# Kernel optimization log

Measured on AMD Instinct MI355X. Metric: run time of the kernel, lower is better.

## Reference

```python
import jax, jax.numpy as jnp
import numpy as np

D_MODEL = 768
D_STATE = 16
D_CONV = 4
EXPAND = 2
N_LAYERS = 8
VOCAB = 512
MAXSEQ = 2048
BATCH = 8
SEQ = 2048
D_INNER = EXPAND * D_MODEL
N_EMO, N_STY, N_KEY, N_MODE = 8, 8, 12, 2


def setup_inputs() -> dict:
    key = jax.random.key(0)
    ks = jax.random.split(key, 32)
    def nrm(k, shape, s=0.02):
        return (jax.random.normal(k, shape) * s).astype(jnp.float32)
    inp = {}
    inp['tokens'] = jax.random.randint(ks[0], (BATCH, SEQ), 0, VOCAB)
    inp['emotion'] = jax.random.randint(ks[1], (BATCH,), 0, N_EMO)
    inp['style'] = jax.random.randint(ks[2], (BATCH,), 0, N_STY)
    inp['key_sig'] = jax.random.randint(ks[3], (BATCH,), 0, N_KEY)
    inp['mode'] = jax.random.randint(ks[4], (BATCH,), 0, N_MODE)
    inp['bpm'] = (jax.random.uniform(ks[5], (BATCH,)) * 140.0 + 60.0).astype(jnp.float32)
    inp['tok_emb'] = nrm(ks[6], (VOCAB, D_MODEL))
    inp['emo_emb'] = nrm(ks[7], (N_EMO, D_MODEL))
    inp['sty_emb'] = nrm(ks[8], (N_STY, D_MODEL))
    inp['key_emb'] = nrm(ks[9], (N_KEY, D_MODEL))
    inp['mode_emb'] = nrm(ks[10], (N_MODE, D_MODEL))
    inp['bpm_w'] = nrm(ks[11], (D_MODEL, 1))
    inp['bpm_b'] = jnp.zeros((D_MODEL,), jnp.float32)
    inp['cond_w'] = nrm(ks[12], (D_MODEL, 5 * D_MODEL))
    inp['cond_b'] = jnp.zeros((D_MODEL,), jnp.float32)
    inp['pos_emb'] = nrm(ks[13], (MAXSEQ, D_MODEL))
    inp['ln_g'] = jnp.ones((N_LAYERS, D_MODEL), jnp.float32)
    inp['ln_b'] = jnp.zeros((N_LAYERS, D_MODEL), jnp.float32)
    inp['in_w'] = nrm(ks[14], (N_LAYERS, 2 * D_INNER, D_MODEL))
    inp['conv_w'] = nrm(ks[15], (N_LAYERS, D_INNER, 1, D_CONV), 0.1)
    inp['xproj_w'] = nrm(ks[16], (N_LAYERS, 2 * D_STATE, D_INNER))
    inp['dt_w'] = nrm(ks[17], (N_LAYERS, D_INNER, D_STATE))
    inp['dt_b'] = jnp.zeros((N_LAYERS, D_INNER), jnp.float32)
    inp['bproj_w'] = nrm(ks[18], (N_LAYERS, D_INNER, D_STATE))
    inp['d_param'] = jnp.ones((N_LAYERS, D_INNER), jnp.float32)
    inp['out_w'] = nrm(ks[19], (N_LAYERS, D_MODEL, D_INNER))
    inp['final_g'] = jnp.ones((D_MODEL,), jnp.float32)
    inp['final_b'] = jnp.zeros((D_MODEL,), jnp.float32)
    inp['head_w'] = nrm(ks[20], (VOCAB, D_MODEL))
    inp['head_b'] = jnp.zeros((VOCAB,), jnp.float32)
    return inp


def _layernorm(x, g, b):
    mu = x.mean(-1, keepdims=True)
    v = ((x - mu) ** 2).mean(-1, keepdims=True)
    return (x - mu) * jax.lax.rsqrt(v + 1e-5) * g + b


def _silu(x):
    return x * jax.nn.sigmoid(x)


def _mamba_block(x, in_w, conv_w, xproj_w, dt_w, dt_b, bproj_w, d_param, out_w):
    B, L, _ = x.shape
    xz = x @ in_w.T                       # [B,L,2*di]
    xc, z = jnp.split(xz, 2, axis=-1)
    # causal depthwise conv1d: torch pads d_conv-1 both sides then slices [:L]
    xt = jnp.transpose(xc, (0, 2, 1))     # [B,di,L]
    xt = jax.lax.conv_general_dilated(xt, conv_w, (1,), [(D_CONV - 1, 0)],
                                      feature_group_count=D_INNER)
    xc = _silu(jnp.transpose(xt, (0, 2, 1)))   # [B,L,di]
    dt_raw, b_raw = jnp.split(xc @ xproj_w.T, 2, axis=-1)  # each [B,L,ds]
    delta = jnp.clip(jax.nn.softplus(dt_raw @ dt_w.T + dt_b), 1e-4, 1.0)  # [B,L,di]
    bp = b_raw @ bproj_w.T                 # [B,L,di]

    def step(h, inputs):
        d, u, bb = inputs
        h = h * (1.0 - d) + u * bb
        return h, h

    xs = (jnp.transpose(delta, (1, 0, 2)),
          jnp.transpose(xc, (1, 0, 2)),
          jnp.transpose(bp, (1, 0, 2)))    # time-major [L,B,di]
    h0 = jnp.zeros((B, D_INNER), x.dtype)
    _, ys = jax.lax.scan(step, h0, xs)
    y = jnp.transpose(ys, (1, 0, 2)) + d_param * xc
    y = y * _silu(z)
    return y @ out_w.T


def reference(tokens, emotion, style, key_sig, mode, bpm, tok_emb, emo_emb, sty_emb,
              key_emb, mode_emb, bpm_w, bpm_b, cond_w, cond_b, pos_emb, ln_g, ln_b,
              in_w, conv_w, xproj_w, dt_w, dt_b, bproj_w, d_param, out_w,
              final_g, final_b, head_w, head_b):
    B, L = tokens.shape
    cond = jnp.concatenate([
        emo_emb[emotion], sty_emb[style], key_emb[key_sig], mode_emb[mode],
        bpm[:, None] @ bpm_w.T + bpm_b], axis=-1)       # [B,5d]
    cond = cond @ cond_w.T + cond_b                      # [B,d]
    x = tok_emb[tokens] + cond[:, None, :] + pos_emb[:L][None]
    for i in range(N_LAYERS):
        res = x
        h = _layernorm(x, ln_g[i], ln_b[i])
        x = res + _mamba_block(h, in_w[i], conv_w[i], xproj_w[i], dt_w[i],
                               dt_b[i], bproj_w[i], d_param[i], out_w[i])
    x = _layernorm(x, final_g, final_b)
    return x @ head_w.T + head_b
```

## Files before the change

kernel.cpp:

```cpp
#include <hip/hip_runtime.h>
#include <cstdint>

#define BATCH 8
#define SEQ   2048
#define DM    768
#define DI    1536
#define DS    16
#define NL    8
#define NVOCAB 512
#define BT    (BATCH*SEQ)
#define NCHUNK 32
#define TC    (SEQ/NCHUNK)

typedef __attribute__((ext_vector_type(8))) short bf16x8;
typedef __attribute__((ext_vector_type(4))) float f32x4;

__device__ __forceinline__ unsigned short f2bf(float f){
  unsigned int u = __float_as_uint(f);
  u += 0x7fffu + ((u >> 16) & 1u);
  return (unsigned short)(u >> 16);
}
__device__ __forceinline__ float bf2f(unsigned short s){
  return __uint_as_float(((unsigned int)s) << 16);
}
__device__ __forceinline__ float sigm(float x){ return 1.0f/(1.0f + __expf(-x)); }
__device__ __forceinline__ float siluf(float x){ return x * sigm(x); }
__device__ __forceinline__ float fast_softplus(float x){
  return (x > 15.0f) ? x : __logf(1.0f + __expf(x));
}
__device__ __forceinline__ void async16(void* l, const void* g){
  __builtin_amdgcn_global_load_lds(
      (const __attribute__((address_space(1))) unsigned int*)g,
      (__attribute__((address_space(3))) unsigned int*)l, 16, 0, 0);
}
__device__ __forceinline__ float dot4(f32x4 a, f32x4 b){
  return fmaf(a[0],b[0], fmaf(a[1],b[1], fmaf(a[2],b[2], a[3]*b[3])));
}

__global__ void cvt_bf16_kernel(const float4* __restrict__ in, ushort4* __restrict__ out, int n4){
  int i = blockIdx.x*256 + threadIdx.x;
  int stride = gridDim.x*256;
  for(; i<n4; i+=stride){
    float4 v = in[i];
    ushort4 o; o.x=f2bf(v.x); o.y=f2bf(v.y); o.z=f2bf(v.z); o.w=f2bf(v.w);
    out[i]=o;
  }
}

__global__ void wcomb_kernel(const float* __restrict__ dt_w, const float* __restrict__ bproj_w,
                             unsigned short* __restrict__ out){
  int idx = blockIdx.x*256 + threadIdx.x;
  int k = idx & 31, ld = idx >> 5;
  float v = (k < 16) ? dt_w[(long)ld*16 + k] : bproj_w[(long)ld*16 + (k-16)];
  out[idx] = f2bf(v);
}

__global__ __launch_bounds__(256) void cond_kernel(const int* __restrict__ emotion,
    const int* __restrict__ style, const int* __restrict__ keysig, const int* __restrict__ modei,
    const float* __restrict__ bpm, const float* __restrict__ emo_emb, const float* __restrict__ sty_emb,
    const float* __restrict__ key_emb, const float* __restrict__ mode_emb,
    const float* __restrict__ bpm_w, const float* __restrict__ bpm_b,
    const float* __restrict__ cond_w, const float* __restrict__ cond_b,
    float* __restrict__ cond_out){
  int b = blockIdx.y;
  int tid = threadIdx.x;
  __shared__ float vec[5*DM];
  int e = emotion[b], st = style[b], ks = keysig[b], md = modei[b];
  float bp = bpm[b];
  for(int j=tid; j<960; j+=256){
    int seg = j/192, o4 = j - seg*192;
    float4 v;
    if(seg==0)      v = reinterpret_cast<const float4*>(emo_emb + (long)e*DM)[o4];
    else if(seg==1) v = reinterpret_cast<const float4*>(sty_emb + (long)st*DM)[o4];
    else if(seg==2) v = reinterpret_cast<const float4*>(key_emb + (long)ks*DM)[o4];
    else if(seg==3) v = reinterpret_cast<const float4*>(mode_emb + (long)md*DM)[o4];
    else {
      float4 w = reinterpret_cast<const float4*>(bpm_w)[o4];
      float4 bb = reinterpret_cast<const float4*>(bpm_b)[o4];
      v = make_float4(fmaf(bp,w.x,bb.x), fmaf(bp,w.y,bb.y), fmaf(bp,w.z,bb.z), fmaf(bp,w.w,bb.w));
    }
    reinterpret_cast<float4*>(vec)[j] = v;
  }
  __syncthreads();
  int wid = tid>>6, lane = tid&63;
  int dm = blockIdx.x*4 + wid;
  const float4* w4 = reinterpret_cast<const float4*>(cond_w + (long)dm*(5*DM));
  const float4* v4 = reinterpret_cast<const float4*>(vec);
  float acc = 0.f;
  #pragma unroll 5
  for(int j=lane; j<960; j+=64){
    float4 w = w4[j], v = v4[j];
    acc = fmaf(w.x,v.x, fmaf(w.y,v.y, fmaf(w.z,v.z, fmaf(w.w,v.w, acc))));
  }
  #pragma unroll
  for(int off=32; off>0; off>>=1) acc += __shfl_xor(acc, off);
  if(lane==0) cond_out[b*DM + dm] = acc + cond_b[dm];
}

__global__ void embed_kernel(const int* __restrict__ tokens, const float* __restrict__ tok_emb,
    const float* __restrict__ cond, const float* __restrict__ pos_emb, float* __restrict__ x){
  int bt = blockIdx.x;
  int b = bt >> 11, t = bt & 2047;
  int tok = tokens[bt];
  const float4* te = reinterpret_cast<const float4*>(tok_emb + (long)tok*DM);
  const float4* ce = reinterpret_cast<const float4*>(cond + (long)b*DM);
  const float4* pe = reinterpret_cast<const float4*>(pos_emb + (long)t*DM);
  float4* xo = reinterpret_cast<float4*>(x + (long)bt*DM);
  int i = threadIdx.x;
  float4 a = te[i], c = ce[i], p = pe[i];
  xo[i] = make_float4(a.x+c.x+p.x, a.y+c.y+p.y, a.z+c.z+p.z, a.w+c.w+p.w);
}

__global__ __launch_bounds__(256) void ln_bf16_kernel(const float* __restrict__ x,
                     const float* __restrict__ g, const float* __restrict__ bta,
                     unsigned short* __restrict__ out){
  int row  = blockIdx.x*4 + (threadIdx.x >> 6);
  int lane = threadIdx.x & 63;
  const float* xr = x + (long)row*DM;
  float4 v[3];
  float sum=0.f, sq=0.f;
  #pragma unroll
  for(int i=0;i<3;i++){
    v[i] = *reinterpret_cast<const float4*>(xr + i*256 + lane*4);
    sum += v[i].x + v[i].y + v[i].z + v[i].w;
    sq  += v[i].x*v[i].x + v[i].y*v[i].y + v[i].z*v[i].z + v[i].w*v[i].w;
  }
  #pragma unroll
  for(int off=32; off>0; off>>=1){
    sum += __shfl_xor(sum, off);
    sq  += __shfl_xor(sq , off);
  }
  float mu  = sum * (1.0f/DM);
  float var = sq  * (1.0f/DM) - mu*mu;
  float rs  = rsqrtf(var + 1e-5f);
  unsigned short* orow = out + (long)row*DM;
  #pragma unroll
  for(int i=0;i<3;i++){
    int d = i*256 + lane*4;
    float4 gg = *reinterpret_cast<const float4*>(g + d);
    float4 bb = *reinterpret_cast<const float4*>(bta + d);
    ushort4 o;
    o.x = f2bf((v[i].x - mu)*rs*gg.x + bb.x);
    o.y = f2bf((v[i].y - mu)*rs*gg.y + bb.y);
    o.z = f2bf((v[i].z - mu)*rs*gg.z + bb.z);
    o.w = f2bf((v[i].w - mu)*rs*gg.w + bb.w);
    *reinterpret_cast<ushort4*>(orow + d) = o;
  }
}

template<int MODE>
__global__ __launch_bounds__(256) void gemm_lds(const unsigned short* __restrict__ A,
                                               const unsigned short* __restrict__ B,
                                               void* __restrict__ Cv,
                                               const float* __restrict__ bias,
                                               int K, int ldc){
  __shared__ short As[128*64];
  __shared__ short Bs[128*64];
  const short* Ap = (const short*)A;
  const short* Bp = (const short*)B;
  int tid  = threadIdx.x;
  int lane = tid & 63;
  int wid  = tid >> 6;

  int nbx = gridDim.x;
  int id  = blockIdx.y*nbx + blockIdx.x;
  int q   = (nbx*gridDim.y) >> 3;
  int swz = (id & 7)*q + (id >> 3);
  int bx  = swz % nbx, by = swz / nbx;
  int row0 = by*128;
  int col0 = bx*128;

  int srow[4], goff[4];
  #pragma unroll
  for(int j=0;j<4;j++){
    int c = j*256 + tid;
    int row = c>>3, s = c&7;
    srow[j] = row;
    goff[j] = (s ^ (row&7))*8;
  }

  int wr = (wid>>1)*64;
  int wc = (wid&1)*64;
  int fr = lane & 15;
  int kq = lane >> 4;
  int fx = fr & 7;

  f32x4 acc[4][4];
  #pragma unroll
  for(int m=0;m<4;m++)
    #pragma unroll
    for(int n=0;n<4;n++)
      acc[m][n] = (f32x4){0.f,0.f,0.f,0.f};

  for(int kt=0; kt<K; kt+=64){
    #pragma unroll
    for(int j=0;j<4;j++){
      int c = j*256 + tid;
      async16((char*)As + c*16, Ap + (long)(row0+srow[j])*K + kt + goff[j]);
      async16((char*)Bs + c*16, Bp + (long)(col0+srow[j])*K + kt + goff[j]);
    }
    __syncthreads();
    #pragma unroll
    for(int ks=0; ks<2; ks++){
      int sA = ((ks*4 + kq) ^ fx) * 8;
      bf16x8 av[4], bv[4];
      #pragma unroll
      for(int m=0;m<4;m++)
        av[m] = *reinterpret_cast<const bf16x8*>(As + (wr + m*16 + fr)*64 + sA);
      #pragma unroll
      for(int n=0;n<4;n++)
        bv[n] = *reinterpret_cast<const bf16x8*>(Bs + (wc + n*16 + fr)*64 + sA);
      #pragma unroll
      for(int m=0;m<4;m++)
        #pragma unroll
        for(int n=0;n<4;n++)
          acc[m][n] = __builtin_amdgcn_mfma_f32_16x16x32_bf16(av[m], bv[n], acc[m][n], 0, 0, 0);
    }
    __syncthreads();
  }

  int rr = (lane >> 4) << 2;
  int cc = lane & 15;
  #pragma unroll
  for(int m=0;m<4;m++){
    #pragma unroll
    for(int n=0;n<4;n++){
      int col = col0 + wc + n*16 + cc;
      #pragma unroll
      for(int i=0;i<4;i++){
        long idx = (long)(row0 + wr + m*16 + rr + i)*ldc + col;
        float v = acc[m][n][i];
        if(MODE==3)      ((unsigned short*)Cv)[idx] = f2bf(v);
        else if(MODE==1) ((float*)Cv)[idx] += v;
        else if(MODE==2) ((float*)Cv)[idx] = v + bias[col];
        else             ((float*)Cv)[idx] = v;
      }
    }
  }
}

__global__ __launch_bounds__(512) void gemm256(const unsigned short* __restrict__ A,
                                               const unsigned short* __restrict__ B,
                                               unsigned short* __restrict__ C,
                                               int K, int ldc){
  __shared__ short smem[2][2][256*64];
  const short* Ap = (const short*)A;
  const short* Bp = (const short*)B;
  int tid  = threadIdx.x;
  int lane = tid & 63;
  int wid  = tid >> 6;

  int nbx = gridDim.x;
  int id  = blockIdx.y*nbx + blockIdx.x;
  int q   = (nbx*gridDim.y) >> 3;
  int swz = (id & 7)*q + (id >> 3);
  int bx  = swz % nbx, by = swz / nbx;
  int row0 = by*256;
  int col0 = bx*256;

  int srow[4], goff[4];
  #pragma unroll
  for(int j=0;j<4;j++){
    int c = j*512 + tid;
    int row = c>>3, s = c&7;
    srow[j] = row;
    goff[j] = (s ^ (row&7))*8;
  }

  int wr = (wid>>2)*128;
  int wc = (wid&3)*64;
  int fr = lane & 15;
  int kq = lane >> 4;
  int fx = fr & 7;

  f32x4 acc[8][4];
  #pragma unroll
  for(int m=0;m<8;m++)
    #pragma unroll
    for(int n=0;n<4;n++)
      acc[m][n] = (f32x4){0.f,0.f,0.f,0.f};

  #define STAGE256(buf, kt) { \
    char* aB = (char*)&smem[buf][0][0]; \
    char* bB = (char*)&smem[buf][1][0]; \
    _Pragma("unroll") \
    for(int j=0;j<4;j++){ \
      int c = j*512 + tid; \
      async16(aB + c*16, Ap + (long)(row0+srow[j])*K + (kt) + goff[j]); \
      async16(bB + c*16, Bp + (long)(col0+srow[j])*K + (kt) + goff[j]); \
    } }

  int NT = K >> 6;
  STAGE256(0, 0)
  for(int t=0; t<NT; ++t){
    int cur = t & 1;
    if(t+1 < NT){
      STAGE256(cur^1, (t+1)*64)
      asm volatile("s_waitcnt vmcnt(8)" ::: "memory");
    } else {
      asm volatile("s_waitcnt vmcnt(0)" ::: "memory");
    }
    __builtin_amdgcn_s_barrier();
    __builtin_amdgcn_sched_barrier(0);
    const short* As = &smem[cur][0][0];
    const short* Bs = &smem[cur][1][0];
    __builtin_amdgcn_s_setprio(1);
    #pragma unroll
    for(int qp=0; qp<4; qp++){
      int qm = qp>>1, qn = qp&1;
      bf16x8 av[4][2], bv[2][2];
      #pragma unroll
      for(int ks=0; ks<2; ks++){
        int sA = ((ks*4 + kq) ^ fx) * 8;
        #pragma unroll
        for(int m4=0;m4<4;m4++)
          av[m4][ks] = *reinterpret_cast<const bf16x8*>(As + (wr + (qm*4+m4)*16 + fr)*64 + sA);
        #pragma unroll
        for(int n2=0;n2<2;n2++)
          bv[n2][ks] = *reinterpret_cast<const bf16x8*>(Bs + (wc + (qn*2+n2)*16 + fr)*64 + sA);
      }
      #pragma unroll
      for(int ks=0; ks<2; ks++)
        #pragma unroll
        for(int m4=0;m4<4;m4++)
          #pragma unroll
          for(int n2=0;n2<2;n2++)
            acc[qm*4+m4][qn*2+n2] = __builtin_amdgcn_mfma_f32_16x16x32_bf16(
                av[m4][ks], bv[n2][ks], acc[qm*4+m4][qn*2+n2], 0, 0, 0);
    }
    __builtin_amdgcn_s_setprio(0);
    __builtin_amdgcn_sched_barrier(0);
    __builtin_amdgcn_s_barrier();
  }
  #undef STAGE256

  int rr = (lane >> 4) << 2;
  int cc = lane & 15;
  #pragma unroll
  for(int m=0;m<8;m++){
    #pragma unroll
    for(int n=0;n<4;n++){
      int col = col0 + wc + n*16 + cc;
      #pragma unroll
      for(int i=0;i<4;i++){
        long idx = (long)(row0 + wr + m*16 + rr + i)*ldc + col;
        C[idx] = f2bf(acc[m][n][i]);
      }
    }
  }
}

__global__ __launch_bounds__(256) void xproj_kernel(const unsigned short* __restrict__ xz,
      const float* __restrict__ cw, const unsigned short* __restrict__ wbf,
      float* __restrict__ dtb){
  __shared__ unsigned short xcs[16][DI+8];
  __shared__ float pdt[4][16][32];
  int blk = blockIdx.x;
  int b  = blk >> 7;
  int t0 = (blk & 127) << 4;
  int tid = threadIdx.x;
  long base = ((long)b*SEQ + t0)*(2*DI);
  if(tid < 192){
    int d0 = tid*8;
    float cc0[8], cc1[8], cc2[8], cc3[8];
    #pragma unroll
    for(int j=0;j<8;j++){
      cc0[j]=cw[(d0+j)*4+0]; cc1[j]=cw[(d0+j)*4+1];
      cc2[j]=cw[(d0+j)*4+2]; cc3[j]=cw[(d0+j)*4+3];
    }
    float wm3[8], wm2[8], wm1[8];
    #pragma unroll
    for(int j=0;j<8;j++){ wm3[j]=0.f; wm2[j]=0.f; wm1[j]=0.f; }
    if(t0>0){
      bf16x8 v3 = *reinterpret_cast<const bf16x8*>(xz + base - 3*(2*DI) + d0);
      bf16x8 v2 = *reinterpret_cast<const bf16x8*>(xz + base - 2*(2*DI) + d0);
      bf16x8 v1 = *reinterpret_cast<const bf16x8*>(xz + base - 1*(2*DI) + d0);
      #pragma unroll
      for(int j=0;j<8;j++){
        wm3[j]=bf2f((unsigned short)v3[j]);
        wm2[j]=bf2f((unsigned short)v2[j]);
        wm1[j]=bf2f((unsigned short)v1[j]);
      }
    }
    for(int tt=0; tt<16; tt++){
      bf16x8 vt = *reinterpret_cast<const bf16x8*>(xz + base + (long)tt*(2*DI) + d0);
      bf16x8 o;
      #pragma unroll
      for(int j=0;j<8;j++){
        float wt = bf2f((unsigned short)vt[j]);
        float u  = cc0[j]*wm3[j] + cc1[j]*wm2[j] + cc2[j]*wm1[j] + cc3[j]*wt;
        o[j] = (short)f2bf(siluf(u));
        wm3[j]=wm2[j]; wm2[j]=wm1[j]; wm1[j]=wt;
      }
      *reinterpret_cast<bf16x8*>(&xcs[tt][d0]) = o;
    }
  }
  __syncthreads();
  int wid = tid >> 6, lane = tid & 63;
  int fr = lane & 15, kq = lane >> 4;
  f32x4 a0 = (f32x4){0.f,0.f,0.f,0.f};
  f32x4 a1 = (f32x4){0.f,0.f,0.f,0.f};
  const unsigned short* w0 = wbf + (long)fr*DI;
  const unsigned short* w1 = wbf + (long)(16+fr)*DI;
  int kbase = wid*384 + kq*8;
  #pragma unroll
  for(int ks=0; ks<12; ks++){
    int k = kbase + ks*32;
    bf16x8 av = *reinterpret_cast<const bf16x8*>(&xcs[fr][k]);
    bf16x8 b0 = *reinterpret_cast<const bf16x8*>(w0 + k);
    bf16x8 b1 = *reinterpret_cast<const bf16x8*>(w1 + k);
    a0 = __builtin_amdgcn_mfma_f32_16x16x32_bf16(av, b0, a0, 0, 0, 0);
    a1 = __builtin_amdgcn_mfma_f32_16x16x32_bf16(av, b1, a1, 0, 0, 0);
  }
  int rr = kq << 2;
  #pragma unroll
  for(int i=0;i<4;i++){
    pdt[wid][rr+i][fr]      = a0[i];
    pdt[wid][rr+i][16+fr]   = a1[i];
  }
  __syncthreads();
  for(int e = tid; e < 512; e += 256){
    int r = e >> 5, s = e & 31;
    float v = pdt[0][r][s] + pdt[1][r][s] + pdt[2][r][s] + pdt[3][r][s];
    dtb[((long)b*SEQ + t0 + r)*32 + s] = v;
  }
}

__global__ __launch_bounds__(256) void scanAY_mfma_kernel(const unsigned short* __restrict__ xz,
      const float* __restrict__ dtb, const float* __restrict__ cw,
      const unsigned short* __restrict__ wcomb,
      const float* __restrict__ dtbias_g, const float* __restrict__ dp_g,
      float2* __restrict__ chunk, unsigned short* __restrict__ y0s,
      unsigned short* __restrict__ as_s){
  __shared__ unsigned short abuf[64][32];
  __shared__ unsigned short dab[64*256*2];
  int c = blockIdx.x, db = blockIdx.y, b = blockIdx.z;
  int tid = threadIdx.x;
  int t0 = c*TC;
  {
    const float4* src = reinterpret_cast<const float4*>(dtb + ((long)b*SEQ + t0)*32);
    float4 v0 = src[tid*2], v1 = src[tid*2+1];
    bf16x8 o;
    o[0]=(short)f2bf(v0.x); o[1]=(short)f2bf(v0.y); o[2]=(short)f2bf(v0.z); o[3]=(short)f2bf(v0.w);
    o[4]=(short)f2bf(v1.x); o[5]=(short)f2bf(v1.y); o[6]=(short)f2bf(v1.z); o[7]=(short)f2bf(v1.w);
    *reinterpret_cast<bf16x8*>(&abuf[tid>>2][(tid&3)*8]) = o;
  }
  __syncthreads();
  {
    int w = tid >> 6, lane = tid & 63;
    int fr = lane & 15, kq = lane >> 4;
    bf16x8 zero = {0,0,0,0,0,0,0,0};
    bf16x8 bq[4], bp[4];
    #pragma unroll
    for(int nt=0; nt<4; nt++){
      int dcol = db*256 + w*64 + nt*16 + fr;
      bf16x8 wv = *reinterpret_cast<const bf16x8*>(wcomb + (long)dcol*32 + kq*8);
      bq[nt] = (kq<2) ? wv : zero;
      bp[nt] = (kq<2) ? zero : wv;
    }
    #pragma unroll
    for(int mt=0; mt<4; mt++){
      bf16x8 av = *reinterpret_cast<const bf16x8*>(&abuf[mt*16 + fr][kq*8]);
      #pragma unroll
      for(int nt=0; nt<4; nt++){
        f32x4 aq = __builtin_amdgcn_mfma_f32_16x16x32_bf16(av, bq[nt], (f32x4){0.f,0.f,0.f,0.f}, 0,0,0);
        f32x4 ap = __builtin_amdgcn_mfma_f32_16x16x32_bf16(av, bp[nt], (f32x4){0.f,0.f,0.f,0.f}, 0,0,0);
        int dl = w*64 + nt*16 + fr;
        #pragma unroll
        for(int i=0;i<4;i++){
          int t = mt*16 + kq*4 + i;
          unsigned int pack = (unsigned int)f2bf(aq[i]) | (((unsigned int)f2bf(ap[i]))<<16);
          *reinterpret_cast<unsigned int*>(&dab[(t*256 + dl)*2]) = pack;
        }
      }
    }
  }
  int d = db*256 + tid;
  float c0=cw[d*4],c1=cw[d*4+1],c2=cw[d*4+2],c3=cw[d*4+3];
  float bias = dtbias_g[d];
  float dp = dp_g[d];
  asm volatile("" : "+v"(c0),"+v"(c1),"+v"(c2),"+v"(c3),"+v"(bias),"+v"(dp));
  long base = ((long)b*SEQ + t0)*(2*DI) + d;
  float wm3 = (t0>0) ? bf2f(xz[base - 3*(2*DI)]) : 0.f;
  float wm2 = (t0>0) ? bf2f(xz[base - 2*(2*DI)]) : 0.f;
  float wm1 = (t0>0) ? bf2f(xz[base - 1*(2*DI)]) : 0.f;
  const unsigned short* xp = xz + base;
  long sidx = ((long)b*SEQ + t0)*DI + d;
  unsigned short* yp = y0s + sidx;
  unsigned short* ap2 = as_s + sidx;
  __syncthreads();
  float h = 0.f, P = 1.f;
  const unsigned int* dab32 = reinterpret_cast<const unsigned int*>(dab);
  for(int g=0; g<TC/8; g++){
    unsigned short xv[8];
    #pragma unroll
    for(int j=0;j<8;j++){ xv[j] = xp[(long)j*2*DI]; }
    xp += 8L*2*DI;
    #pragma unroll
    for(int j=0;j<8;j++){
      float wt = bf2f(xv[j]);
      float u = siluf(fmaf(c3,wt, fmaf(c2,wm1, fmaf(c1,wm2, c0*wm3))));
      wm3=wm2; wm2=wm1; wm1=wt;
      unsigned int pk = dab32[(g*8+j)*256 + tid];
      float da = bias + bf2f((unsigned short)(pk & 0xffffu));
      float ba = bf2f((unsigned short)(pk >> 16));
      float delta = fminf(fmaxf(fast_softplus(da), 1e-4f), 1.0f);
      float a = 1.0f - delta;
      h = fmaf(h, a, u*ba);
      P *= a;
      yp[(long)j*DI]  = f2bf(fmaf(dp, u, h));
      ap2[(long)j*DI] = f2bf(P);
    }
    yp += 8L*DI; ap2 += 8L*DI;
  }
  chunk[((long)b*DI + d)*NCHUNK + c] = make_float2(P, h);
}

__global__ __launch_bounds__(256) void scanAY_kernel(const unsigned short* __restrict__ xz,
      const float* __restrict__ dtb, const float* __restrict__ cw,
      const float* __restrict__ dtw_g, const float* __restrict__ dtbias_g,
      const float* __restrict__ bpw_g, const float* __restrict__ dp_g,
      float2* __restrict__ chunk, unsigned short* __restrict__ y,
      unsigned short* __restrict__ asz_s){
  __shared__ float dsb[TC*32];
  int c = blockIdx.x, db = blockIdx.y, b = blockIdx.z;
  int d = db*256 + threadIdx.x;
  int t0 = c*TC;
  {
    const float4* src = reinterpret_cast<const float4*>(dtb + ((long)b*SEQ + t0)*32);
    float4* dst = reinterpret_cast<float4*>(dsb);
    dst[threadIdx.x]       = src[threadIdx.x];
    dst[threadIdx.x + 256] = src[threadIdx.x + 256];
  }
  float c0=cw[d*4],c1=cw[d*4+1],c2=cw[d*4+2],c3=cw[d*4+3];
  f32x4 wq0 = *reinterpret_cast<const f32x4*>(dtw_g + d*16 + 0);
  f32x4 wq1 = *reinterpret_cast<const f32x4*>(dtw_g + d*16 + 4);
  f32x4 wq2 = *reinterpret_cast<const f32x4*>(dtw_g + d*16 + 8);
  f32x4 wq3 = *reinterpret_cast<const f32x4*>(dtw_g + d*16 + 12);
  f32x4 wp0 = *reinterpret_cast<const f32x4*>(bpw_g + d*16 + 0);
  f32x4 wp1 = *reinterpret_cast<const f32x4*>(bpw_g + d*16 + 4);
  f32x4 wp2 = *reinterpret_cast<const f32x4*>(bpw_g + d*16 + 8);
  f32x4 wp3 = *reinterpret_cast<const f32x4*>(bpw_g + d*16 + 12);
  float bias = dtbias_g[d];
  float dp = dp_g[d];
  asm volatile("" : "+v"(wq0),"+v"(wq1),"+v"(wq2),"+v"(wq3),
                    "+v"(wp0),"+v"(wp1),"+v"(wp2),"+v"(wp3),
                    "+v"(c0),"+v"(c1),"+v"(c2),"+v"(c3),"+v"(bias),"+v"(dp));
  long base = ((long)b*SEQ + t0)*(2*DI) + d;
  float wm3 = (t0>0) ? bf2f(xz[base - 3*(2*DI)]) : 0.f;
  float wm2 = (t0>0) ? bf2f(xz[base - 2*(2*DI)]) : 0.f;
  float wm1 = (t0>0) ? bf2f(xz[base - 1*(2*DI)]) : 0.f;
  const unsigned short* xp = xz + base;
  const unsigned short* zp = xz + base + DI;
  long sidx = ((long)b*SEQ + t0)*DI + d;
  unsigned short* yp = y + sidx;
  unsigned short* ap = asz_s + sidx;
  __syncthreads();
  float h = 0.f, P = 1.f;
  for(int g=0; g<TC/8; g++){
    unsigned short xv[8], zv[8];
    #pragma unroll
    for(int j=0;j<8;j++){ xv[j] = xp[(long)j*2*DI]; zv[j] = zp[(long)j*2*DI]; }
    xp += 8L*2*DI; zp += 8L*2*DI;
    const float* rp = dsb + g*8*32;
    #pragma unroll
    for(int j=0;j<8;j++){
      float wt = bf2f(xv[j]);
      float u = siluf(fmaf(c3,wt, fmaf(c2,wm1, fmaf(c1,wm2, c0*wm3))));
      wm3=wm2; wm2=wm1; wm1=wt;
      const f32x4* row = reinterpret_cast<const f32x4*>(rp + j*32);
      float da = bias + dot4(row[0],wq0) + dot4(row[1],wq1) + dot4(row[2],wq2) + dot4(row[3],wq3);
      float ba =        dot4(row[4],wp0) + dot4(row[5],wp1) + dot4(row[6],wp2) + dot4(row[7],wp3);
      float delta = fminf(fmaxf(fast_softplus(da), 1e-4f), 1.0f);
      float a = 1.0f - delta;
      h = fmaf(h, a, u*ba);
      P *= a;
      float sz = siluf(bf2f(zv[j]));
      yp[(long)j*DI] = f2bf(fmaf(dp, u, h) * sz);
      ap[(long)j*DI] = f2bf(P * sz);
    }
    yp += 8L*DI; ap += 8L*DI;
  }
  chunk[((long)b*DI + d)*NCHUNK + c] = make_float2(P, h);
}

__global__ __launch_bounds__(256) void h0_kernel(const float2* __restrict__ chunk,
                                                 float* __restrict__ h0tab){
  int idx = blockIdx.x*256 + threadIdx.x;
  int b = idx / DI, d = idx - b*DI;
  const float2* cb = chunk + ((long)b*DI + d)*NCHUNK;
  float h0 = 0.f;
  for(int c=0; c<NCHUNK; c++){
    h0tab[((long)b*NCHUNK + c)*DI + d] = h0;
    float2 ps = cb[c];
    h0 = fmaf(ps.x, h0, ps.y);
  }
}

__global__ __launch_bounds__(256) void fixup_z_kernel(const unsigned short* __restrict__ as_s,
      const float* __restrict__ h0tab, const unsigned short* __restrict__ xz,
      unsigned short* __restrict__ y){
  int i = (blockIdx.x*256 + threadIdx.x)*8;
  int bt = i / DI;
  int d  = i - bt*DI;
  int b  = bt >> 11;
  int c  = (bt & 2047) >> 6;
  const float* hp = h0tab + ((long)b*NCHUNK + c)*DI + d;
  f32x4 h0a = *reinterpret_cast<const f32x4*>(hp);
  f32x4 h0b = *reinterpret_cast<const f32x4*>(hp + 4);
  bf16x8 yv = *reinterpret_cast<const bf16x8*>(y + i);
  bf16x8 av = *reinterpret_cast<const bf16x8*>(as_s + i);
  bf16x8 zv = *reinterpret_cast<const bf16x8*>(xz + (long)bt*(2*DI) + DI + d);
  bf16x8 o;
  #pragma unroll
  for(int j=0;j<8;j++){
    float h0 = (j<4) ? h0a[j] : h0b[j-4];
    float v = fmaf(h0, bf2f((unsigned short)av[j]), bf2f((unsigned short)yv[j]));
    o[j] = (short)f2bf(v * siluf(bf2f((unsigned short)zv[j])));
  }
  *reinterpret_cast<bf16x8*>(y + i) = o;
}

__global__ __launch_bounds__(256) void fixup_kernel(const unsigned short* __restrict__ asz_s,
      const float* __restrict__ h0tab, unsigned short* __restrict__ y){
  int i = (blockIdx.x*256 + threadIdx.x)*8;
  int bt = i / DI;
  int d  = i - bt*DI;
  int b  = bt >> 11;
  int c  = (bt & 2047) >> 6;
  const float* hp = h0tab + ((long)b*NCHUNK + c)*DI + d;
  f32x4 h0a = *reinterpret_cast<const f32x4*>(hp);
  f32x4 h0b = *reinterpret_cast<const f32x4*>(hp + 4);
  bf16x8 yv = *reinterpret_cast<const bf16x8*>(y + i);
  bf16x8 av = *reinterpret_cast<const bf16x8*>(asz_s + i);
  bf16x8 o;
  #pragma unroll
  for(int j=0;j<8;j++){
    float h0 = (j<4) ? h0a[j] : h0b[j-4];
    o[j] = (short)f2bf(fmaf(h0, bf2f((unsigned short)av[j]), bf2f((unsigned short)yv[j])));
  }
  *reinterpret_cast<bf16x8*>(y + i) = o;
}

extern "C" void kernel_launch(void* const* d_in, const int* in_sizes, int n_in,
                              void* d_out, int out_size, void* d_ws, size_t ws_size,
                              hipStream_t stream){
  const int*   tokens  = (const int*)  d_in[0];
  const int*   emotion = (const int*)  d_in[1];
  const int*   style   = (const int*)  d_in[2];
  const int*   keysig  = (const int*)  d_in[3];
  const int*   modei   = (const int*)  d_in[4];
  const float* bpm     = (const float*)d_in[5];
  const float* tok_emb = (const float*)d_in[6];
  const float* emo_emb = (const float*)d_in[7];
  const float* sty_emb = (const float*)d_in[8];
  const float* key_emb = (const float*)d_in[9];
  const float* mode_emb= (const float*)d_in[10];
  const float* bpm_w   = (const float*)d_in[11];
  const float* bpm_b   = (const float*)d_in[12];
  const float* cond_w  = (const float*)d_in[13];
  const float* cond_b  = (const float*)d_in[14];
  const float* pos_emb = (const float*)d_in[15];
  const float* ln_g    = (const float*)d_in[16];
  const float* ln_b    = (const float*)d_in[17];
  const float* in_w    = (const float*)d_in[18];
  const float* conv_w  = (const float*)d_in[19];
  const float* xproj_w = (const float*)d_in[20];
  const float* dt_w    = (const float*)d_in[21];
  const float* dt_b    = (const float*)d_in[22];
  const float* bproj_w = (const float*)d_in[23];
  const float* d_param = (const float*)d_in[24];
  const float* out_w   = (const float*)d_in[25];
  const float* final_g = (const float*)d_in[26];
  const float* final_b = (const float*)d_in[27];
  const float* head_w  = (const float*)d_in[28];
  const float* head_b  = (const float*)d_in[29];

  char* ws = (char*)d_ws;
  float*          x       = (float*)(ws + 0L);
  unsigned short* hy      = (unsigned short*)(ws + 50331648L);
  unsigned short* xz      = (unsigned short*)(ws + 100663296L);
  float*          dtbuf   = (float*)(ws + 201326592L);
  float2*         chunk   = (float2*)(ws + 203423744L);
  float*          condv   = (float*)(ws + 206569472L);
  unsigned short* inwb    = (unsigned short*)(ws + 206594048L);
  unsigned short* outwb   = (unsigned short*)(ws + 211312640L);
  unsigned short* headwb  = (unsigned short*)(ws + 213671936L);
  unsigned short* wbf_all = (unsigned short*)(ws + 214458368L);
  float*          h0tab   = (float*)(ws + 215244800L);
  unsigned short* asz_s   = (unsigned short*)(ws + 216817664L);
  unsigned short* wcombb  = (unsigned short*)(ws + 267149312L);

  const bool use_mfma = (ws_size >= 267935744UL);

  unsigned short* h_bf = hy;
  unsigned short* y_bf = hy;
  unsigned short* xfin = hy;

  cvt_bf16_kernel<<<128,256,0,stream>>>((const float4*)head_w,(ushort4*)headwb, NVOCAB*DM/4);
  cvt_bf16_kernel<<<384,256,0,stream>>>((const float4*)xproj_w,(ushort4*)wbf_all, NL*32*DI/4);
  if(use_mfma)
    wcomb_kernel<<<NL*DI*32/256,256,0,stream>>>(dt_w, bproj_w, wcombb);
  cond_kernel<<<dim3(DM/4,8),256,0,stream>>>(emotion, style, keysig, modei, bpm, emo_emb, sty_emb,
        key_emb, mode_emb, bpm_w, bpm_b, cond_w, cond_b, condv);
  embed_kernel<<<BT,192,0,stream>>>(tokens, tok_emb, condv, pos_emb, x);

  for(int l=0; l<NL; l++){
    cvt_bf16_kernel<<<1024,256,0,stream>>>((const float4*)(in_w  + (long)l*2*DI*DM), (ushort4*)inwb,  2*DI*DM/4);
    cvt_bf16_kernel<<<512, 256,0,stream>>>((const float4*)(out_w + (long)l*DM*DI),   (ushort4*)outwb, DM*DI/4);
    ln_bf16_kernel<<<BT/4,256,0,stream>>>(x, ln_g + l*DM, ln_b + l*DM, h_bf);
    gemm256<<<dim3(2*DI/256, BT/256),512,0,stream>>>(h_bf, inwb, xz, DM, 2*DI);
    xproj_kernel<<<BT/16,256,0,stream>>>(xz, conv_w + l*DI*4, wbf_all + (long)l*32*DI, dtbuf);
    if(use_mfma){
      scanAY_mfma_kernel<<<dim3(NCHUNK,6,BATCH),256,0,stream>>>(xz, dtbuf, conv_w + l*DI*4,
            wcombb + (long)l*DI*32, dt_b + l*DI, d_param + l*DI, chunk, y_bf, asz_s);
      h0_kernel<<<48,256,0,stream>>>(chunk, h0tab);
      fixup_z_kernel<<<BT*DI/(256*8),256,0,stream>>>(asz_s, h0tab, xz, y_bf);
    } else {
      scanAY_kernel<<<dim3(NCHUNK,6,BATCH),256,0,stream>>>(xz, dtbuf, conv_w + l*DI*4,
            dt_w + l*DI*DS, dt_b + l*DI, bproj_w + l*DI*DS, d_param + l*DI, chunk, y_bf, asz_s);
      h0_kernel<<<48,256,0,stream>>>(chunk, h0tab);
      fixup_kernel<<<BT*DI/(256*8),256,0,stream>>>(asz_s, h0tab, y_bf);
    }
    gemm_lds<1><<<dim3(DM/128, BT/128),256,0,stream>>>(y_bf, outwb, x, nullptr, DI, DM);
  }
  ln_bf16_kernel<<<BT/4,256,0,stream>>>(x, final_g, final_b, xfin);
  gemm_lds<2><<<dim3(NVOCAB/128, BT/128),256,0,stream>>>(xfin, headwb, d_out, head_b, DM, NVOCAB);
}
```

Baseline: 2.307 ms.

## Use 256x256 MFMA GEMM for out-projection with accumulate epilogue

Templates the 256x256 bf16 MFMA GEMM on an output mode so it can either write bf16 or accumulate into fp32. The residual out-projection GEMM now uses it instead of the 128x128 LDS GEMM. The inner k-step loop is also restructured to load all A/B fragments at once before issuing the MFMAs. This aims for more data reuse per tile, but the out-projection grid shrinks to 192 blocks, fewer than the CU count, and the fragment loading raises register pressure.

```diff
diff --git a/kernel.cpp b/kernel.cpp
--- a/kernel.cpp
+++ b/kernel.cpp
@@ -239,9 +239,10 @@
   }
 }
 
+template<int MODE>
 __global__ __launch_bounds__(512) void gemm256(const unsigned short* __restrict__ A,
                                                const unsigned short* __restrict__ B,
-                                               unsigned short* __restrict__ C,
+                                               void* __restrict__ Cv,
                                                int K, int ldc){
   __shared__ short smem[2][2][256*64];
   const short* Ap = (const short*)A;
@@ -306,27 +307,20 @@
     const short* Bs = &smem[cur][1][0];
     __builtin_amdgcn_s_setprio(1);
     #pragma unroll
-    for(int qp=0; qp<4; qp++){
-      int qm = qp>>1, qn = qp&1;
-      bf16x8 av[4][2], bv[2][2];
-      #pragma unroll
-      for(int ks=0; ks<2; ks++){
-        int sA = ((ks*4 + kq) ^ fx) * 8;
+    for(int ks=0; ks<2; ks++){
+      int sA = ((ks*4 + kq) ^ fx) * 8;
+      bf16x8 av[8], bv[4];
+      #pragma unroll
+      for(int m=0;m<8;m++)
+        av[m] = *reinterpret_cast<const bf16x8*>(As + (wr + m*16 + fr)*64 + sA);
+      #pragma unroll
+      for(int n=0;n<4;n++)
+        bv[n] = *reinterpret_cast<const bf16x8*>(Bs + (wc + n*16 + fr)*64 + sA);
+      #pragma unroll
+      for(int m=0;m<8;m++)
         #pragma unroll
-        for(int m4=0;m4<4;m4++)
-          av[m4][ks] = *reinterpret_cast<const bf16x8*>(As + (wr + (qm*4+m4)*16 + fr)*64 + sA);
-        #pragma unroll
-        for(int n2=0;n2<2;n2++)
-          bv[n2][ks] = *reinterpret_cast<const bf16x8*>(Bs + (wc + (qn*2+n2)*16 + fr)*64 + sA);
-      }
-      #pragma unroll
-      for(int ks=0; ks<2; ks++)
-        #pragma unroll
-        for(int m4=0;m4<4;m4++)
-          #pragma unroll
-          for(int n2=0;n2<2;n2++)
-            acc[qm*4+m4][qn*2+n2] = __builtin_amdgcn_mfma_f32_16x16x32_bf16(
-                av[m4][ks], bv[n2][ks], acc[qm*4+m4][qn*2+n2], 0, 0, 0);
+        for(int n=0;n<4;n++)
+          acc[m][n] = __builtin_amdgcn_mfma_f32_16x16x32_bf16(av[m], bv[n], acc[m][n], 0, 0, 0);
     }
     __builtin_amdgcn_s_setprio(0);
     __builtin_amdgcn_sched_barrier(0);
@@ -344,7 +338,8 @@
       #pragma unroll
       for(int i=0;i<4;i++){
         long idx = (long)(row0 + wr + m*16 + rr + i)*ldc + col;
-        C[idx] = f2bf(acc[m][n][i]);
+        if(MODE==3) ((unsigned short*)Cv)[idx] = f2bf(acc[m][n][i]);
+        else        ((float*)Cv)[idx] += acc[m][n][i];
       }
     }
   }
@@ -709,7 +704,7 @@
     cvt_bf16_kernel<<<1024,256,0,stream>>>((const float4*)(in_w  + (long)l*2*DI*DM), (ushort4*)inwb,  2*DI*DM/4);
     cvt_bf16_kernel<<<512, 256,0,stream>>>((const float4*)(out_w + (long)l*DM*DI),   (ushort4*)outwb, DM*DI/4);
     ln_bf16_kernel<<<BT/4,256,0,stream>>>(x, ln_g + l*DM, ln_b + l*DM, h_bf);
-    gemm256<<<dim3(2*DI/256, BT/256),512,0,stream>>>(h_bf, inwb, xz, DM, 2*DI);
+    gemm256<3><<<dim3(2*DI/256, BT/256),512,0,stream>>>(h_bf, inwb, xz, DM, 2*DI);
     xproj_kernel<<<BT/16,256,0,stream>>>(xz, conv_w + l*DI*4, wbf_all + (long)l*32*DI, dtbuf);
     if(use_mfma){
       scanAY_mfma_kernel<<<dim3(NCHUNK,6,BATCH),256,0,stream>>>(xz, dtbuf, conv_w + l*DI*4,
@@ -722,7 +717,7 @@
       h0_kernel<<<48,256,0,stream>>>(chunk, h0tab);
       fixup_kernel<<<BT*DI/(256*8),256,0,stream>>>(asz_s, h0tab, y_bf);
     }
-    gemm_lds<1><<<dim3(DM/128, BT/128),256,0,stream>>>(y_bf, outwb, x, nullptr, DI, DM);
+    gemm256<1><<<dim3(DM/256, BT/256),512,0,stream>>>(y_bf, outwb, x, DI, DM);
   }
   ln_bf16_kernel<<<BT/4,256,0,stream>>>(x, final_g, final_b, xfin);
   gemm_lds<2><<<dim3(NVOCAB/128, BT/128),256,0,stream>>>(xfin, headwb, d_out, head_b, DM, NVOCAB);
```

After: 2.426 ms. 1.05x slower.
